# Kernel tuning notes

Measured on AMD Instinct MI355X. Metric: run time of the kernel, lower is better.

The kernel has to match this reference:

```python
import jax, jax.numpy as jnp
import numpy as np

N = 50000
NEG_SLOPE = 0.2


def leaky_relu(x, slope=NEG_SLOPE):
    return jnp.where(x >= 0, x, slope * x)


def gat_conv(x, edge_index, W, a_src, a_dst, bias):
    """PyG GATConv, heads=1, add_self_loops=True.
    x: [N, Fin], edge_index: [2, E] (row 0 = source j, row 1 = target i),
    W: [Fin, Fout], a_src/a_dst: [Fout], bias: [Fout].
    """
    n = x.shape[0]
    # add self loops
    loops = jnp.arange(n, dtype=edge_index.dtype)
    src = jnp.concatenate([edge_index[0], loops])
    dst = jnp.concatenate([edge_index[1], loops])

    xw = x @ W                       # [N, Fout]
    alpha_src = xw @ a_src           # [N]
    alpha_dst = xw @ a_dst           # [N]

    e = leaky_relu(alpha_src[src] + alpha_dst[dst])   # [E+N]
    # segment softmax over edges sharing the same target node
    m = jax.ops.segment_max(e, dst, num_segments=n)   # [N]
    ex = jnp.exp(e - m[dst])
    denom = jax.ops.segment_sum(ex, dst, num_segments=n)  # [N] (>0 via self loops)
    att = ex / denom[dst]                              # [E+N]

    msgs = att[:, None] * xw[src]                      # [E+N, Fout]
    out = jax.ops.segment_sum(msgs, dst, num_segments=n)
    return out + bias


def setup_inputs() -> dict:
    key = jax.random.key(0)
    ks = jax.random.split(key, 12)
    E = 800000
    Fin, H, Fout = 128, 256, 128
    x = jax.random.normal(ks[0], (N, Fin), dtype=jnp.float32)
    edge_index = jax.random.randint(ks[1], (2, E), 0, N, dtype=jnp.int64)
    s = 0.1
    W1 = jax.random.normal(ks[2], (Fin, H), dtype=jnp.float32) * s
    a1_src = jax.random.normal(ks[3], (H,), dtype=jnp.float32) * s
    a1_dst = jax.random.normal(ks[4], (H,), dtype=jnp.float32) * s
    b1 = jax.random.normal(ks[5], (H,), dtype=jnp.float32) * s
    W2 = jax.random.normal(ks[6], (H, Fout), dtype=jnp.float32) * s
    a2_src = jax.random.normal(ks[7], (Fout,), dtype=jnp.float32) * s
    a2_dst = jax.random.normal(ks[8], (Fout,), dtype=jnp.float32) * s
    b2 = jax.random.normal(ks[9], (Fout,), dtype=jnp.float32) * s
    return {"x": x, "edge_index": edge_index, "W1": W1, "a1_src": a1_src,
            "a1_dst": a1_dst, "b1": b1, "W2": W2, "a2_src": a2_src,
            "a2_dst": a2_dst, "b2": b2}


def reference(x, edge_index, W1, a1_src, a1_dst, b1, W2, a2_src, a2_dst, b2):
    h = jax.nn.relu(gat_conv(x, edge_index, W1, a1_src, a1_dst, b1))
    return gat_conv(h, edge_index, W2, a2_src, a2_dst, b2)
```

## Files before the change

kernel.cpp:

```cpp
#include <hip/hip_runtime.h>
#include <hip/hip_bf16.h>

typedef __attribute__((ext_vector_type(8))) short short8;
typedef __attribute__((ext_vector_type(4))) float floatx4;

#define CAP 8192
#define BIN_CH 2048

__device__ __forceinline__ float read_f(const void* p, long long i, int fp32m) {
  return fp32m ? ((const float*)p)[i] : (float)((const __hip_bfloat16*)p)[i];
}
__device__ __forceinline__ float bf2f(unsigned short u) {
  return __uint_as_float((unsigned)u << 16);
}
__device__ __forceinline__ unsigned short f2bf(float f) {
  const unsigned u = __float_as_uint(f);
  return (unsigned short)((u + 0x7fffu + ((u >> 16) & 1u)) >> 16);
}

__device__ __forceinline__ void pack_one(const void* W, unsigned short* Wp, int i,
                                         int K, int NOUT, int m) {
  const int k = i / NOUT, n = i - k * NOUT;
  const int ct = n >> 4, c = n & 15, ks = k >> 5, quad = (k >> 3) & 3, j = k & 7;
  Wp[(((ct * (K / 32) + ks) * 4 + quad) * 16 + c) * 8 + j] = f2bf(read_f(W, i, m));
}

__global__ __launch_bounds__(256) void prep_k(const void* __restrict__ x,
                                              const void* __restrict__ ei,
                                              const void* __restrict__ W1,
                                              const void* __restrict__ a1s,
                                              const void* __restrict__ a1d,
                                              const void* __restrict__ b1,
                                              const void* __restrict__ W2,
                                              const void* __restrict__ a2s,
                                              const void* __restrict__ a2d,
                                              const void* __restrict__ b2,
                                              unsigned short* __restrict__ Wp1,
                                              unsigned short* __restrict__ Wp2,
                                              float* __restrict__ w_as1, float* __restrict__ w_ad1,
                                              float* __restrict__ v_a2s, float* __restrict__ v_a2d,
                                              float* __restrict__ v_b1,  float* __restrict__ v_b2,
                                              int* __restrict__ bkcnt,
                                              int* __restrict__ flags) {
  __shared__ int fl_s[2];
  const int t = threadIdx.x, b = blockIdx.x;
  if (t < 64) {
    const unsigned short w = ((const unsigned short*)x)[t * 2];
    const int ef = (w >> 7) & 0xff;
    const bool bf_ok = (ef >= 90 && ef <= 140);
    const unsigned hi = ((const unsigned*)ei)[t * 2 + 1];
    const unsigned long long bm = __ballot(bf_ok);
    const unsigned long long zm = __ballot(hi == 0u);
    if (t == 0) {
      fl_s[0] = (bm == ~0ull) ? 0 : 1;
      fl_s[1] = (zm == ~0ull) ? 1 : 0;
      if (b == 0) { flags[0] = fl_s[0]; flags[1] = fl_s[1]; }
    }
  }
  __syncthreads();
  const int m = fl_s[0];

  if (b < 128) {
    pack_one(W1, Wp1, b * 256 + t, 128, 256, m);
  } else if (b < 256) {
    pack_one(W2, Wp2, (b - 128) * 256 + t, 256, 128, m);
  } else if (b == 256) {
    if (t < 128) {
      float sa = 0.f, sb = 0.f;
      for (int j = 0; j < 256; ++j) {
        const float w = read_f(W1, (long long)t * 256 + j, m);
        sa = fmaf(w, read_f(a1s, j, m), sa);
        sb = fmaf(w, read_f(a1d, j, m), sb);
      }
      w_as1[t] = sa;
      w_ad1[t] = sb;
    }
  } else if (b == 257) {
    if (t < 128) v_a2s[t] = read_f(a2s, t, m);
    else         v_a2d[t - 128] = read_f(a2d, t - 128, m);
  } else if (b == 258) {
    v_b1[t] = read_f(b1, t, m);
  } else {
    if (t < 128) v_b2[t] = read_f(b2, t, m);
    bkcnt[t] = 0;
  }
}

__global__ __launch_bounds__(256) void canon_alpha_k(const void* __restrict__ x,
                                                     const float* __restrict__ was,
                                                     const float* __restrict__ wad,
                                                     unsigned short* __restrict__ xb,
                                                     float* __restrict__ as_, float* __restrict__ ad_,
                                                     int n, const int* __restrict__ flags) {
  const int gid = blockIdx.x * 256 + threadIdx.x;
  const int node = gid >> 6, lane = gid & 63;
  if (node >= n) return;
  const int m = flags[0];
  const long long base = (long long)node * 128 + lane * 2;
  const float v0 = read_f(x, base, m), v1 = read_f(x, base + 1, m);
  ushort2 q;
  q.x = f2bf(v0); q.y = f2bf(v1);
  *(ushort2*)(xb + base) = q;
  float s1 = fmaf(v0, was[lane * 2], v1 * was[lane * 2 + 1]);
  float s2 = fmaf(v0, wad[lane * 2], v1 * wad[lane * 2 + 1]);
  for (int off = 32; off; off >>= 1) {
    s1 += __shfl_down(s1, off);
    s2 += __shfl_down(s2, off);
  }
  if (lane == 0) { as_[node] = s1; ad_[node] = s2; }
}

__device__ __forceinline__ void edge_sd(const void* ei, int e, int E, int i64m, int n,
                                        int& s, int& d) {
  if (e < E) {
    if (i64m) { s = (int)((const long long*)ei)[e]; d = (int)((const long long*)ei)[E + e]; }
    else      { s = ((const int*)ei)[e];            d = ((const int*)ei)[E + e]; }
  } else { s = d = e - E; }
  s = min(max(s, 0), n - 1);
  d = min(max(d, 0), n - 1);
}

__global__ __launch_bounds__(256) void bin_k(const void* __restrict__ ei,
                                             unsigned* __restrict__ bpool,
                                             int* __restrict__ bkcnt,
                                             int E, int EN, int n,
                                             const int* __restrict__ flags) {
  __shared__ unsigned stage[BIN_CH];
  __shared__ unsigned daddr[BIN_CH];
  __shared__ int bcnt_s[256], boff_s[256], gbase_s[256], sd[256];
  __shared__ int vtot_s;
  const int t = threadIdx.x;
  const int c0 = blockIdx.x * BIN_CH;
  const int i64m = flags[1];
  bcnt_s[t] = 0;
  __syncthreads();

  unsigned val[BIN_CH / 256];
  int buk[BIN_CH / 256];
#pragma unroll
  for (int i = 0; i < BIN_CH / 256; ++i) {
    const int e = c0 + i * 256 + t;
    if (e < EN) {
      int s, d;
      edge_sd(ei, e, E, i64m, n, s, d);
      buk[i] = d >> 8;
      val[i] = (unsigned)s | ((unsigned)(d & 255) << 16);
      atomicAdd(&bcnt_s[buk[i]], 1);
    } else buk[i] = -1;
  }
  __syncthreads();

  const int c = bcnt_s[t];
  sd[t] = c;
  __syncthreads();
  for (int off = 1; off < 256; off <<= 1) {
    const int v = (t >= off) ? sd[t - off] : 0;
    __syncthreads();
    sd[t] += v;
    __syncthreads();
  }
  boff_s[t] = sd[t] - c;
  if (t == 255) vtot_s = sd[255];
  gbase_s[t] = (c > 0) ? atomicAdd(&bkcnt[t], c) : 0;
  bcnt_s[t] = 0;
  __syncthreads();

#pragma unroll
  for (int i = 0; i < BIN_CH / 256; ++i) {
    if (buk[i] >= 0) {
      const int lp = atomicAdd(&bcnt_s[buk[i]], 1);
      const int si = boff_s[buk[i]] + lp;
      stage[si] = val[i];
      const int gp = gbase_s[buk[i]] + lp;
      daddr[si] = (gp < CAP) ? (unsigned)(buk[i] * CAP + gp) : 0xFFFFFFFFu;
    }
  }
  __syncthreads();

  const int vt = vtot_s;
  for (int idx = t; idx < vt; idx += 256)
    if (daddr[idx] != 0xFFFFFFFFu) bpool[daddr[idx]] = stage[idx];
}

__global__ __launch_bounds__(256) void bucket_csr_k(const unsigned* __restrict__ bpool,
                                                    const int* __restrict__ bkcnt,
                                                    unsigned short* __restrict__ csrc,
                                                    int* __restrict__ start_g,
                                                    int* __restrict__ deg_g, int n) {
  __shared__ int deg_s[256], cur_s[256], sd[256];
  const int t = threadIdx.x, b = blockIdx.x;
  int cnt = bkcnt[b];
  if (cnt > CAP) cnt = CAP;
  deg_s[t] = 0;
  __syncthreads();
  for (int idx = t; idx < cnt; idx += 256) {
    const unsigned v = bpool[b * CAP + idx];
    atomicAdd(&deg_s[(v >> 16) & 255], 1);
  }
  __syncthreads();
  const int dg = deg_s[t];
  sd[t] = dg;
  __syncthreads();
  for (int off = 1; off < 256; off <<= 1) {
    const int v = (t >= off) ? sd[t - off] : 0;
    __syncthreads();
    sd[t] += v;
    __syncthreads();
  }
  const int excl = sd[t] - dg;
  const int node = b * 256 + t;
  if (node < n) { start_g[node] = b * CAP + excl; deg_g[node] = dg; }
  cur_s[t] = excl;
  __syncthreads();
  for (int idx = t; idx < cnt; idx += 256) {
    const unsigned v = bpool[b * CAP + idx];
    const int p = atomicAdd(&cur_s[(v >> 16) & 255], 1);
    csrc[b * CAP + p] = (unsigned short)(v & 0xFFFFu);
  }
}

__device__ __forceinline__ void agg_node(const int start, const int end,
                                         const unsigned short* __restrict__ csrc,
                                         const float* __restrict__ as_, const float adv,
                                         const unsigned short* __restrict__ xw,
                                         const int lane, float* acc) {
  const int slot = lane >> 4, col = lane & 15;
  float dsum = 0.f;
#pragma unroll
  for (int c = 0; c < 8; ++c) acc[c] = 0.f;

  for (int base = start; base < end; base += 64) {
    const int idx = base + lane;
    int s_pre = 0;
    float w_pre = 0.f;
    if (idx < end) {
      s_pre = (int)csrc[idx];
      float v = as_[s_pre] + adv;
      v = (v >= 0.f) ? v : 0.2f * v;
      w_pre = __expf(fminf(v, 60.f));
    }
    dsum += w_pre;
    const int cnt = min(64, end - base);
    for (int j = 0; j < cnt; j += 8) {
      const int jj0 = j + slot, jj1 = j + 4 + slot;
      int s0 = __shfl(s_pre, jj0);
      float w0 = __shfl(w_pre, jj0);
      int s1 = __shfl(s_pre, jj1);
      float w1 = __shfl(w_pre, jj1);
      const bool ok0 = (jj0 < cnt), ok1 = (jj1 < cnt);
      s0 = ok0 ? s0 : 0; w0 = ok0 ? w0 : 0.f;
      s1 = ok1 ? s1 : 0; w1 = ok1 ? w1 : 0.f;
      const short8 q0 = *(const short8*)(xw + (size_t)s0 * 128 + col * 8);
      const short8 q1 = *(const short8*)(xw + (size_t)s1 * 128 + col * 8);
#pragma unroll
      for (int c = 0; c < 8; ++c) {
        acc[c] = fmaf(w0, bf2f((unsigned short)q0[c]), acc[c]);
        acc[c] = fmaf(w1, bf2f((unsigned short)q1[c]), acc[c]);
      }
    }
  }
  for (int off = 32; off; off >>= 1) dsum += __shfl_down(dsum, off);
  dsum = __shfl(dsum, 0);
  const float r = 1.f / fmaxf(dsum, 1e-30f);
#pragma unroll
  for (int c = 0; c < 8; ++c) {
    acc[c] += __shfl_xor(acc[c], 16);
    acc[c] += __shfl_xor(acc[c], 32);
    acc[c] *= r;
  }
}

#define LSTR 136
__global__ __launch_bounds__(1024) void agg_gemm1_k(const int* __restrict__ start_g,
                                                    const int* __restrict__ deg_g,
                                                    const unsigned short* __restrict__ csrc,
                                                    const float* __restrict__ as_,
                                                    const float* __restrict__ ad_,
                                                    const unsigned short* __restrict__ xb,
                                                    const unsigned short* __restrict__ Wp1,
                                                    const float* __restrict__ v_b1,
                                                    unsigned short* __restrict__ H, int n) {
  __shared__ unsigned short lds[16 * LSTR];
  const int wv = threadIdx.x >> 6, lane = threadIdx.x & 63;
  const int slot = lane >> 4, col = lane & 15;
  const int node = blockIdx.x * 16 + wv;

  float acc[8];
  if (node < n) {
    const int start = start_g[node];
    agg_node(start, start + deg_g[node], csrc, as_, ad_[node], xb, lane, acc);
  } else {
#pragma unroll
    for (int c = 0; c < 8; ++c) acc[c] = 0.f;
  }
  if (slot == 0) {
    short8 q;
#pragma unroll
    for (int c = 0; c < 8; ++c) q[c] = (short)f2bf(acc[c]);
    *(short8*)&lds[wv * LSTR + col * 8] = q;
  }
  __syncthreads();

  const int quad = slot, c = col;
  floatx4 g = {0.f, 0.f, 0.f, 0.f};
#pragma unroll
  for (int ks = 0; ks < 4; ++ks) {
    const short8 af = *(const short8*)&lds[c * LSTR + ks * 32 + quad * 8];
    const short8 bf = *(const short8*)(Wp1 + (size_t)((wv * 4 + ks) * 64 + lane) * 8);
    g = __builtin_amdgcn_mfma_f32_16x16x32_bf16(af, bf, g, 0, 0, 0);
  }
  const float bv = v_b1[wv * 16 + c];
  const int row0 = blockIdx.x * 16;
#pragma unroll
  for (int r = 0; r < 4; ++r) {
    const int rr = row0 + quad * 4 + r;
    const float v = g[r] + bv;
    if (rr < n) H[(size_t)rr * 256 + wv * 16 + c] = f2bf(v > 0.f ? v : 0.f);
  }
}

template<int K, int NOUT>
__global__ __launch_bounds__(256) void gemm_mfma_k(const unsigned short* __restrict__ A,
                                                   const unsigned short* __restrict__ Wp,
                                                   unsigned short* __restrict__ outp,
                                                   const float* __restrict__ av_src,
                                                   const float* __restrict__ av_dst,
                                                   float* __restrict__ as_, float* __restrict__ ad_,
                                                   int nrows) {
  constexpr int KS = K / 32;
  constexpr int CT = NOUT / 16;
  const int wave = threadIdx.x >> 6, lane = threadIdx.x & 63;
  const int quad = lane >> 4, c = lane & 15;
  const int row0 = (blockIdx.x * 4 + wave) * 16;
  if (row0 >= nrows) return;
  int arow = row0 + c;
  if (arow >= nrows) arow = nrows - 1;

  short8 afrag[KS];
  const unsigned short* Ab = A + (size_t)arow * K;
#pragma unroll
  for (int ks = 0; ks < KS; ++ks)
    afrag[ks] = *(const short8*)(Ab + ks * 32 + quad * 8);

  float pa_s[4] = {0.f, 0.f, 0.f, 0.f}, pa_d[4] = {0.f, 0.f, 0.f, 0.f};
#pragma unroll
  for (int ct = 0; ct < CT; ++ct) {
    floatx4 acc = {0.f, 0.f, 0.f, 0.f};
#pragma unroll
    for (int ks = 0; ks < KS; ++ks) {
      const short8 bfrag = *(const short8*)(Wp + (size_t)((ct * KS + ks) * 64 + lane) * 8);
      acc = __builtin_amdgcn_mfma_f32_16x16x32_bf16(afrag[ks], bfrag, acc, 0, 0, 0);
    }
    const float asv = av_src[ct * 16 + c], adv = av_dst[ct * 16 + c];
#pragma unroll
    for (int r = 0; r < 4; ++r) {
      const int rr = row0 + quad * 4 + r;
      pa_s[r] = fmaf(acc[r], asv, pa_s[r]);
      pa_d[r] = fmaf(acc[r], adv, pa_d[r]);
      if (rr < nrows) outp[(size_t)rr * NOUT + ct * 16 + c] = f2bf(acc[r]);
    }
  }
  for (int off = 1; off < 16; off <<= 1) {
#pragma unroll
    for (int r = 0; r < 4; ++r) {
      pa_s[r] += __shfl_xor(pa_s[r], off);
      pa_d[r] += __shfl_xor(pa_d[r], off);
    }
  }
  if (c == 0) {
#pragma unroll
    for (int r = 0; r < 4; ++r) {
      const int rr = row0 + quad * 4 + r;
      if (rr < nrows) { as_[rr] = pa_s[r]; ad_[rr] = pa_d[r]; }
    }
  }
}

__global__ __launch_bounds__(256) void agg_out_k(const int* __restrict__ start_g,
                                                 const int* __restrict__ deg_g,
                                                 const unsigned short* __restrict__ csrc,
                                                 const float* __restrict__ as_,
                                                 const float* __restrict__ ad_,
                                                 const unsigned short* __restrict__ xw,
                                                 const float* __restrict__ bias,
                                                 void* __restrict__ outp, int n,
                                                 const int* __restrict__ flags) {
  const int gid = blockIdx.x * 256 + threadIdx.x;
  const int node = gid >> 6, lane = gid & 63;
  if (node >= n) return;
  const int slot = lane >> 4, col = lane & 15;
  const int start = start_g[node];
  float acc[8];
  agg_node(start, start + deg_g[node], csrc, as_, ad_[node], xw, lane, acc);
  if (slot == 0) {
    const int c0 = col * 8;
    if (flags[0]) {
      float* o = (float*)outp + (size_t)node * 128 + c0;
      floatx4 q0, q1;
#pragma unroll
      for (int c = 0; c < 4; ++c) {
        q0[c] = acc[c] + bias[c0 + c];
        q1[c] = acc[c + 4] + bias[c0 + 4 + c];
      }
      *(floatx4*)o = q0;
      *(floatx4*)(o + 4) = q1;
    } else {
      short8 q;
#pragma unroll
      for (int c = 0; c < 8; ++c) q[c] = (short)f2bf(acc[c] + bias[c0 + c]);
      *(short8*)((unsigned short*)outp + (size_t)node * 128 + c0) = q;
    }
  }
}

extern "C" void kernel_launch(void* const* d_in, const int* in_sizes, int n_in,
                              void* d_out, int out_size, void* d_ws, size_t ws_size,
                              hipStream_t stream) {
  const void* x   = d_in[0];
  const void* ei  = d_in[1];
  const void* W1  = d_in[2];
  const void* a1s = d_in[3];
  const void* a1d = d_in[4];
  const void* b1  = d_in[5];
  const void* W2  = d_in[6];
  const void* a2s = d_in[7];
  const void* a2d = d_in[8];
  const void* b2  = d_in[9];

  const int N  = in_sizes[0] / 128;
  const int E  = in_sizes[1] / 2;
  const int EN = E + N;
  const int NBUK = (N + 255) / 256;

  unsigned short* B1 = (unsigned short*)d_ws;
  unsigned short* H  = B1 + (size_t)N * 128;
  float* as_   = (float*)(H + (size_t)N * 256);
  float* ad_   = as_ + N;
  int*   start_g = (int*)(ad_ + N);
  int*   deg_g   = start_g + N;
  int*   bkcnt   = deg_g + N;
  unsigned* bpool = (unsigned*)(bkcnt + 256);
  unsigned short* csrc = (unsigned short*)(bpool + (size_t)NBUK * CAP);
  unsigned short* Wp1 = csrc + (size_t)NBUK * CAP;
  unsigned short* Wp2 = Wp1 + 128 * 256;
  float* vecs  = (float*)(Wp2 + 256 * 128);
  int*   flags = (int*)(vecs + 1152);
  float* w_as1 = vecs,        *w_ad1 = vecs + 128;
  float* v_a2s = vecs + 256,  *v_a2d = vecs + 384;
  float* v_b1  = vecs + 512,  *v_b2  = vecs + 768;

  const int NB = (N * 64 + 255) / 256;
  const int BB = (EN + BIN_CH - 1) / BIN_CH;
  const int MB = (N + 63) / 64;
  const int AG = (N + 15) / 16;

  prep_k<<<260, 256, 0, stream>>>(x, ei, W1, a1s, a1d, b1, W2, a2s, a2d, b2,
                                  Wp1, Wp2, w_as1, w_ad1, v_a2s, v_a2d, v_b1, v_b2,
                                  bkcnt, flags);

  canon_alpha_k<<<NB, 256, 0, stream>>>(x, w_as1, w_ad1, B1, as_, ad_, N, flags);

  bin_k<<<BB, 256, 0, stream>>>(ei, bpool, bkcnt, E, EN, N, flags);
  bucket_csr_k<<<NBUK, 256, 0, stream>>>(bpool, bkcnt, csrc, start_g, deg_g, N);

  agg_gemm1_k<<<AG, 1024, 0, stream>>>(start_g, deg_g, csrc, as_, ad_, B1, Wp1, v_b1, H, N);

  gemm_mfma_k<256, 128><<<MB, 256, 0, stream>>>(H, Wp2, B1, v_a2s, v_a2d, as_, ad_, N);
  agg_out_k<<<NB, 256, 0, stream>>>(start_g, deg_g, csrc, as_, ad_, B1, v_b2, d_out, N, flags);
}
```

Baseline: 261.2 us.

## Fuse layer-2 GEMM and attention logits into aggregation+GEMM1 kernel via LDS

```diff
diff --git a/kernel.cpp b/kernel.cpp
--- a/kernel.cpp
+++ b/kernel.cpp
@@ -271,16 +271,24 @@
 }
 
 #define LSTR 136
-__global__ __launch_bounds__(1024) void agg_gemm1_k(const int* __restrict__ start_g,
-                                                    const int* __restrict__ deg_g,
-                                                    const unsigned short* __restrict__ csrc,
-                                                    const float* __restrict__ as_,
-                                                    const float* __restrict__ ad_,
-                                                    const unsigned short* __restrict__ xb,
-                                                    const unsigned short* __restrict__ Wp1,
-                                                    const float* __restrict__ v_b1,
-                                                    unsigned short* __restrict__ H, int n) {
+#define HSTR 264
+__global__ __launch_bounds__(1024) void agg_gemm12_k(const int* __restrict__ start_g,
+                                                     const int* __restrict__ deg_g,
+                                                     const unsigned short* __restrict__ csrc,
+                                                     const float* __restrict__ as_,
+                                                     const float* __restrict__ ad_,
+                                                     const unsigned short* __restrict__ xb,
+                                                     const unsigned short* __restrict__ Wp1,
+                                                     const unsigned short* __restrict__ Wp2,
+                                                     const float* __restrict__ v_b1,
+                                                     const float* __restrict__ v_a2s,
+                                                     const float* __restrict__ v_a2d,
+                                                     unsigned short* __restrict__ xw2,
+                                                     float* __restrict__ as2,
+                                                     float* __restrict__ ad2, int n) {
   __shared__ unsigned short lds[16 * LSTR];
+  __shared__ unsigned short hs[16 * HSTR];
+  __shared__ float al_s[16], al_d[16];
   const int wv = threadIdx.x >> 6, lane = threadIdx.x & 63;
   const int slot = lane >> 4, col = lane & 15;
   const int node = blockIdx.x * 16 + wv;
@@ -310,69 +318,51 @@
     g = __builtin_amdgcn_mfma_f32_16x16x32_bf16(af, bf, g, 0, 0, 0);
   }
   const float bv = v_b1[wv * 16 + c];
+#pragma unroll
+  for (int r = 0; r < 4; ++r) {
+    const float v = g[r] + bv;
+    hs[(quad * 4 + r) * HSTR + wv * 16 + c] = f2bf(v > 0.f ? v : 0.f);
+  }
+  if (threadIdx.x < 16) { al_s[threadIdx.x] = 0.f; al_d[threadIdx.x] = 0.f; }
+  __syncthreads();
+
   const int row0 = blockIdx.x * 16;
-#pragma unroll
-  for (int r = 0; r < 4; ++r) {
-    const int rr = row0 + quad * 4 + r;
-    const float v = g[r] + bv;
-    if (rr < n) H[(size_t)rr * 256 + wv * 16 + c] = f2bf(v > 0.f ? v : 0.f);
-  }
-}
-
-template<int K, int NOUT>
-__global__ __launch_bounds__(256) void gemm_mfma_k(const unsigned short* __restrict__ A,
-                                                   const unsigned short* __restrict__ Wp,
-                                                   unsigned short* __restrict__ outp,
-                                                   const float* __restrict__ av_src,
-                                                   const float* __restrict__ av_dst,
-                                                   float* __restrict__ as_, float* __restrict__ ad_,
-                                                   int nrows) {
-  constexpr int KS = K / 32;
-  constexpr int CT = NOUT / 16;
-  const int wave = threadIdx.x >> 6, lane = threadIdx.x & 63;
-  const int quad = lane >> 4, c = lane & 15;
-  const int row0 = (blockIdx.x * 4 + wave) * 16;
-  if (row0 >= nrows) return;
-  int arow = row0 + c;
-  if (arow >= nrows) arow = nrows - 1;
-
-  short8 afrag[KS];
-  const unsigned short* Ab = A + (size_t)arow * K;
-#pragma unroll
-  for (int ks = 0; ks < KS; ++ks)
-    afrag[ks] = *(const short8*)(Ab + ks * 32 + quad * 8);
-
-  float pa_s[4] = {0.f, 0.f, 0.f, 0.f}, pa_d[4] = {0.f, 0.f, 0.f, 0.f};
-#pragma unroll
-  for (int ct = 0; ct < CT; ++ct) {
-    floatx4 acc = {0.f, 0.f, 0.f, 0.f};
-#pragma unroll
-    for (int ks = 0; ks < KS; ++ks) {
-      const short8 bfrag = *(const short8*)(Wp + (size_t)((ct * KS + ks) * 64 + lane) * 8);
-      acc = __builtin_amdgcn_mfma_f32_16x16x32_bf16(afrag[ks], bfrag, acc, 0, 0, 0);
-    }
-    const float asv = av_src[ct * 16 + c], adv = av_dst[ct * 16 + c];
+  if (wv < 8) {
+    floatx4 a2 = {0.f, 0.f, 0.f, 0.f};
+#pragma unroll
+    for (int ks = 0; ks < 8; ++ks) {
+      const short8 af = *(const short8*)&hs[c * HSTR + ks * 32 + quad * 8];
+      const short8 bf = *(const short8*)(Wp2 + (size_t)((wv * 8 + ks) * 64 + lane) * 8);
+      a2 = __builtin_amdgcn_mfma_f32_16x16x32_bf16(af, bf, a2, 0, 0, 0);
+    }
+    const float asv = v_a2s[wv * 16 + c], adv = v_a2d[wv * 16 + c];
+    float pa_s[4], pa_d[4];
 #pragma unroll
     for (int r = 0; r < 4; ++r) {
+      pa_s[r] = a2[r] * asv;
+      pa_d[r] = a2[r] * adv;
       const int rr = row0 + quad * 4 + r;
-      pa_s[r] = fmaf(acc[r], asv, pa_s[r]);
-      pa_d[r] = fmaf(acc[r], adv, pa_d[r]);
-      if (rr < nrows) outp[(size_t)rr * NOUT + ct * 16 + c] = f2bf(acc[r]);
-    }
-  }
-  for (int off = 1; off < 16; off <<= 1) {
-#pragma unroll
-    for (int r = 0; r < 4; ++r) {
-      pa_s[r] += __shfl_xor(pa_s[r], off);
-      pa_d[r] += __shfl_xor(pa_d[r], off);
-    }
-  }
-  if (c == 0) {
-#pragma unroll
-    for (int r = 0; r < 4; ++r) {
-      const int rr = row0 + quad * 4 + r;
-      if (rr < nrows) { as_[rr] = pa_s[r]; ad_[rr] = pa_d[r]; }
-    }
+      if (rr < n) xw2[(size_t)rr * 128 + wv * 16 + c] = f2bf(a2[r]);
+    }
+    for (int off = 1; off < 16; off <<= 1) {
+#pragma unroll
+      for (int r = 0; r < 4; ++r) {
+        pa_s[r] += __shfl_xor(pa_s[r], off);
+        pa_d[r] += __shfl_xor(pa_d[r], off);
+      }
+    }
+    if (c == 0) {
+#pragma unroll
+      for (int r = 0; r < 4; ++r) {
+        atomicAdd(&al_s[quad * 4 + r], pa_s[r]);
+        atomicAdd(&al_d[quad * 4 + r], pa_d[r]);
+      }
+    }
+  }
+  __syncthreads();
+  if (threadIdx.x < 16) {
+    const int rr = row0 + threadIdx.x;
+    if (rr < n) { as2[rr] = al_s[threadIdx.x]; ad2[rr] = al_d[threadIdx.x]; }
   }
 }
 
@@ -434,6 +424,9 @@
 
   unsigned short* B1 = (unsigned short*)d_ws;
   unsigned short* H  = B1 + (size_t)N * 128;
+  unsigned short* xw2 = H;
+  float* as2 = (float*)(H + (size_t)N * 128);
+  float* ad2 = as2 + N;
   float* as_   = (float*)(H + (size_t)N * 256);
   float* ad_   = as_ + N;
   int*   start_g = (int*)(ad_ + N);
@@ -451,7 +444,6 @@
 
   const int NB = (N * 64 + 255) / 256;
   const int BB = (EN + BIN_CH - 1) / BIN_CH;
-  const int MB = (N + 63) / 64;
   const int AG = (N + 15) / 16;
 
   prep_k<<<260, 256, 0, stream>>>(x, ei, W1, a1s, a1d, b1, W2, a2s, a2d, b2,
@@ -463,8 +455,8 @@
   bin_k<<<BB, 256, 0, stream>>>(ei, bpool, bkcnt, E, EN, N, flags);
   bucket_csr_k<<<NBUK, 256, 0, stream>>>(bpool, bkcnt, csrc, start_g, deg_g, N);
 
-  agg_gemm1_k<<<AG, 1024, 0, stream>>>(start_g, deg_g, csrc, as_, ad_, B1, Wp1, v_b1, H, N);
-
-  gemm_mfma_k<256, 128><<<MB, 256, 0, stream>>>(H, Wp2, B1, v_a2s, v_a2d, as_, ad_, N);
-  agg_out_k<<<NB, 256, 0, stream>>>(start_g, deg_g, csrc, as_, ad_, B1, v_b2, d_out, N, flags);
-}
+  agg_gemm12_k<<<AG, 1024, 0, stream>>>(start_g, deg_g, csrc, as_, ad_, B1, Wp1, Wp2,
+                                        v_b1, v_a2s, v_a2d, xw2, as2, ad2, N);
+
+  agg_out_k<<<NB, 256, 0, stream>>>(start_g, deg_g, csrc, as2, ad2, xw2, v_b2, d_out, N, flags);
+}
```

Result: no change. 256.7 us (-1.7%).
